# Optimization experiments

Hardware: AMD Instinct MI355X
Metric: run time of the kernel (lower is better)

The kernel has to match this reference:

```python
import jax, jax.numpy as jnp
import numpy as np

B, S, D, H, DOUT = 4, 2048, 1024, 4, 1024


def setup_inputs() -> dict:
    key = jax.random.key(0)
    ks = jax.random.split(key, 11)
    x = jax.random.normal(ks[0], (B, S, D), dtype=jnp.float32)
    phase = jax.random.normal(ks[1], (H, D), dtype=jnp.float32) * 0.02
    sc = 1.0 / np.sqrt(D)
    Wq = jax.random.normal(ks[2], (D, H * D), dtype=jnp.float32) * sc
    bq = jnp.zeros((H * D,), dtype=jnp.float32)
    Wk = jax.random.normal(ks[3], (D, H * D), dtype=jnp.float32) * sc
    bk = jnp.zeros((H * D,), dtype=jnp.float32)
    Wv = jax.random.normal(ks[4], (D, H * D), dtype=jnp.float32) * sc
    bv = jnp.zeros((H * D,), dtype=jnp.float32)
    Wo = jax.random.normal(ks[5], (H * D, DOUT), dtype=jnp.float32) / np.sqrt(H * D)
    bo = jnp.zeros((DOUT,), dtype=jnp.float32)
    return {"x": x, "phase": phase, "Wq": Wq, "bq": bq, "Wk": Wk, "bk": bk,
            "Wv": Wv, "bv": bv, "Wo": Wo, "bo": bo}


def reference(x, phase, Wq, bq, Wk, bk, Wv, bv, Wo, bo):
    b, s, d = x.shape
    h = phase.shape[0]
    q = (x @ Wq + bq).reshape(b, s, h, d)  # [B,S,H,D]
    k = (x @ Wk + bk).reshape(b, s, h, d)
    v = (x @ Wv + bv).reshape(b, s, h, d)
    # q *= e^{i phase}; k *= e^{-i phase}; scores = Re(q @ k^T) over last dim.
    # Re( e^{i p1} e^{-i p2} ) = cos(p1)cos(p2) + sin(p1)sin(p2), so use real pairs.
    c, sn = jnp.cos(phase), jnp.sin(phase)  # [H,D]
    qr, qi = q * c, q * sn
    kr, ki = k * c, k * sn
    scale = 1.0 / np.sqrt(d)
    # per-position head-vs-head scores: [B,S,H,H]
    scores = (jnp.einsum('bshd,bsgd->bshg', qr, kr)
              + jnp.einsum('bshd,bsgd->bshg', qi, ki)) * scale
    attn = jax.nn.softmax(scores, axis=-1)  # dropout is identity in eval
    out = jnp.einsum('bshg,bsgd->bshd', attn, v)  # [B,S,H,D]
    # replicate torch: transpose(1,2) -> [B,H,S,D] then view [B,S,H*D]
    out = jnp.swapaxes(out, 1, 2).reshape(b, s, h * d)
    return out @ Wo + bo
```

## Files before the change

kernel.cpp:

```cpp
#include <hip/hip_runtime.h>
#include <hip/hip_bf16.h>
#include <stdint.h>

#define DEVI __device__ __forceinline__

using f32x4  = __attribute__((ext_vector_type(4))) float;
using bf16x8 = __attribute__((ext_vector_type(8))) short;

DEVI ushort f2bf(float f) {
  union { float f; uint32_t u; } v; v.f = f;
  uint32_t u = v.u;
  uint32_t r = (u + 0x7fffu + ((u >> 16) & 1u)) >> 16;
  return (ushort)r;
}
DEVI float bf2f(ushort h) {
  union { uint32_t u; float f; } v; v.u = ((uint32_t)h) << 16;
  return v.f;
}

__global__ void k_cast_bf16(const float* __restrict__ in, ushort* __restrict__ out, int n8) {
  int i = blockIdx.x * blockDim.x + threadIdx.x;
  if (i >= n8) return;
  const float4* in4 = reinterpret_cast<const float4*>(in);
  float4 a = in4[i * 2], b = in4[i * 2 + 1];
  uint4 o;
  o.x = (uint32_t)f2bf(a.x) | ((uint32_t)f2bf(a.y) << 16);
  o.y = (uint32_t)f2bf(a.z) | ((uint32_t)f2bf(a.w) << 16);
  o.z = (uint32_t)f2bf(b.x) | ((uint32_t)f2bf(b.y) << 16);
  o.w = (uint32_t)f2bf(b.z) | ((uint32_t)f2bf(b.w) << 16);
  reinterpret_cast<uint4*>(out)[i] = o;
}

__global__ __launch_bounds__(256)
void k_transpose_cast(const float* __restrict__ in, ushort* __restrict__ out, int R, int C) {
  __shared__ float tile[64][65];
  int c0 = blockIdx.x * 64, r0 = blockIdx.y * 64;
  int t = threadIdx.x, tr = t >> 6, tc = t & 63;
#pragma unroll
  for (int i = 0; i < 16; ++i) {
    int r = i * 4 + tr;
    tile[r][tc] = in[(size_t)(r0 + r) * C + c0 + tc];
  }
  __syncthreads();
#pragma unroll
  for (int i = 0; i < 16; ++i) {
    int rr = i * 4 + tr;
    out[(size_t)(c0 + rr) * R + r0 + tc] = f2bf(tile[tc][rr]);
  }
}

__global__ void k_phase(const float* __restrict__ p, float* __restrict__ c,
                        float* __restrict__ s, int n) {
  int i = blockIdx.x * blockDim.x + threadIdx.x;
  if (i < n) { float v = p[i]; c[i] = cosf(v); s[i] = sinf(v); }
}

__global__ void k_concat3(const float* __restrict__ a, const float* __restrict__ b,
                          const float* __restrict__ c, float* __restrict__ o, int n) {
  int i = blockIdx.x * blockDim.x + threadIdx.x;
  if (i < n) { o[i] = a[i]; o[i + n] = b[i]; o[i + 2 * n] = c[i]; }
}

DEVI void glds16(const ushort* g, ushort* l) {
  __builtin_amdgcn_global_load_lds(
      (const __attribute__((address_space(1))) void*)g,
      (__attribute__((address_space(3))) void*)l, 16, 0, 0);
}

template <typename OutT>
__global__ __launch_bounds__(512, 2)
void k_gemm256(const ushort* __restrict__ A, const ushort* __restrict__ Bt,
               const float* __restrict__ bias, OutT* __restrict__ C,
               int M, int N, int K) {
  __shared__ ushort lds[3 * 16384];

  int nbx = N >> 8;
  int nwg = gridDim.x, orig = blockIdx.x;
  int bm, bn;
  if ((nbx & 7) == 0 && nbx >= 16 && (nwg & 7) == 0) {
    int xcd = orig & 7, idx = orig >> 3, sw2 = nbx >> 3;
    bm = idx / sw2;
    bn = xcd * sw2 + idx % sw2;
  } else {
    int q = nwg >> 3, r8 = nwg & 7;
    int xcd = orig & 7, idx = orig >> 3;
    int swz = (xcd < r8 ? xcd * (q + 1) : r8 * (q + 1) + (xcd - r8) * q) + idx;
    bm = swz / nbx; bn = swz % nbx;
  }

  int t = threadIdx.x;
  int lane = t & 63, wid = t >> 6;
  int wm = wid >> 2, wn = wid & 3;
  int fr = lane & 15, fq = lane >> 4;
  int spR = fq ^ ((fr >> 1) & 3);

  int rl  = t >> 2;
  int spW = (t & 3) ^ ((rl >> 1) & 3);
  const ushort* aS0 = A  + (size_t)(bm * 256 + rl) * K + spW * 8;
  const ushort* aS1 = aS0 + (size_t)128 * K;
  const ushort* bS0 = Bt + (size_t)(bn * 256 + rl) * K + spW * 8;
  const ushort* bS1 = bS0 + (size_t)128 * K;
  ushort* ldsw = lds + wid * 512;

  f32x4 acc[8][4] = {};
  int NT = K >> 5;

  glds16(aS0,      ldsw);
  glds16(aS1,      ldsw + 4096);
  glds16(bS0,      ldsw + 8192);
  glds16(bS1,      ldsw + 12288);
  glds16(aS0 + 32, ldsw + 16384);
  glds16(aS1 + 32, ldsw + 16384 + 4096);
  glds16(bS0 + 32, ldsw + 16384 + 8192);
  glds16(bS1 + 32, ldsw + 16384 + 12288);
  asm volatile("s_waitcnt vmcnt(4)" ::: "memory");
  __builtin_amdgcn_s_barrier();
  __builtin_amdgcn_sched_barrier(0);

  int iA0 = (wm * 128 + fr) * 4 + spR;
  int iB0 = (wn * 64 + fr) * 4 + spR;

  for (int kt = 0; kt < NT; ++kt) {
    if (kt + 2 < NT) {
      ushort* lb = lds + ((kt + 2) % 3) * 16384 + wid * 512;
      int ko = (kt + 2) * 32;
      glds16(aS0 + ko, lb);
      glds16(aS1 + ko, lb + 4096);
      glds16(bS0 + ko, lb + 8192);
      glds16(bS1 + ko, lb + 12288);
    }
    const bf16x8* Av = reinterpret_cast<const bf16x8*>(lds + (kt % 3) * 16384);
    const bf16x8* Bv = Av + 1024;

    bf16x8 bfr[4];
#pragma unroll
    for (int nt = 0; nt < 4; ++nt) bfr[nt] = Bv[iB0 + nt * 64];

#pragma unroll
    for (int mi = 0; mi < 2; ++mi) {
      bf16x8 af[4];
#pragma unroll
      for (int m4 = 0; m4 < 4; ++m4) af[m4] = Av[iA0 + (mi * 4 + m4) * 64];
      __builtin_amdgcn_s_setprio(1);
#pragma unroll
      for (int m4 = 0; m4 < 4; ++m4)
#pragma unroll
        for (int nt = 0; nt < 4; ++nt)
          acc[mi * 4 + m4][nt] =
              __builtin_amdgcn_mfma_f32_16x16x32_bf16(af[m4], bfr[nt], acc[mi * 4 + m4][nt], 0, 0, 0);
      __builtin_amdgcn_s_setprio(0);
    }

    if (kt + 1 < NT) {
      if (kt + 2 < NT) { asm volatile("s_waitcnt vmcnt(4)" ::: "memory"); }
      else             { asm volatile("s_waitcnt vmcnt(0)" ::: "memory"); }
      __builtin_amdgcn_s_barrier();
      __builtin_amdgcn_sched_barrier(0);
    }
  }

#pragma unroll
  for (int mt = 0; mt < 8; ++mt)
#pragma unroll
    for (int nt = 0; nt < 4; ++nt) {
      int col = bn * 256 + wn * 64 + nt * 16 + fr;
      float bb = bias[col];
#pragma unroll
      for (int i = 0; i < 4; ++i) {
        int row = bm * 256 + wm * 128 + mt * 16 + fq * 4 + i;
        float v = acc[mt][nt][i] + bb;
        size_t off = (size_t)row * N + col;
        if constexpr (sizeof(OutT) == 2) C[off] = f2bf(v);
        else                             C[off] = v;
      }
    }
}

template <typename OutT>
__global__ __launch_bounds__(512, 2)
void k_gemm_n128(const ushort* __restrict__ A, const ushort* __restrict__ Bt,
                 const float* __restrict__ bias, OutT* __restrict__ C,
                 int M, int N, int K) {
  __shared__ ushort lds[3 * 12288];

  int nbx = N >> 7;
  int nwg = gridDim.x, orig = blockIdx.x;
  int q = nwg >> 3, r8 = nwg & 7;
  int xcd = orig & 7, idx = orig >> 3;
  int swz = (xcd < r8 ? xcd * (q + 1) : r8 * (q + 1) + (xcd - r8) * q) + idx;
  int bm = swz / nbx, bn = swz % nbx;

  int t = threadIdx.x;
  int lane = t & 63, wid = t >> 6;
  int wm = wid >> 1, wn = wid & 1;
  int fr = lane & 15, fq = lane >> 4;
  int spR = fq ^ ((fr >> 1) & 3);

  int rl  = t >> 2;
  int spW = (t & 3) ^ ((rl >> 1) & 3);
  const ushort* aS0 = A  + (size_t)(bm * 256 + rl) * K + spW * 8;
  const ushort* aS1 = aS0 + (size_t)128 * K;
  const ushort* bS0 = Bt + (size_t)(bn * 128 + rl) * K + spW * 8;
  ushort* ldsw = lds + wid * 512;

  f32x4 acc[4][4] = {};
  int NT = K >> 5;

  glds16(aS0,      ldsw);
  glds16(aS1,      ldsw + 4096);
  glds16(bS0,      ldsw + 8192);
  glds16(aS0 + 32, ldsw + 12288);
  glds16(aS1 + 32, ldsw + 12288 + 4096);
  glds16(bS0 + 32, ldsw + 12288 + 8192);
  asm volatile("s_waitcnt vmcnt(3)" ::: "memory");
  __builtin_amdgcn_s_barrier();
  __builtin_amdgcn_sched_barrier(0);

  int iA0 = (wm * 64 + fr) * 4 + spR;
  int iB0 = (wn * 64 + fr) * 4 + spR;

  for (int kt = 0; kt < NT; ++kt) {
    if (kt + 2 < NT) {
      ushort* lb = lds + ((kt + 2) % 3) * 12288 + wid * 512;
      int ko = (kt + 2) * 32;
      glds16(aS0 + ko, lb);
      glds16(aS1 + ko, lb + 4096);
      glds16(bS0 + ko, lb + 8192);
    }
    const bf16x8* Av = reinterpret_cast<const bf16x8*>(lds + (kt % 3) * 12288);
    const bf16x8* Bv = Av + 1024;

    bf16x8 bfr[4], af[4];
#pragma unroll
    for (int nt = 0; nt < 4; ++nt) bfr[nt] = Bv[iB0 + nt * 64];
#pragma unroll
    for (int m4 = 0; m4 < 4; ++m4) af[m4] = Av[iA0 + m4 * 64];
    __builtin_amdgcn_s_setprio(1);
#pragma unroll
    for (int m4 = 0; m4 < 4; ++m4)
#pragma unroll
      for (int nt = 0; nt < 4; ++nt)
        acc[m4][nt] = __builtin_amdgcn_mfma_f32_16x16x32_bf16(af[m4], bfr[nt], acc[m4][nt], 0, 0, 0);
    __builtin_amdgcn_s_setprio(0);

    if (kt + 1 < NT) {
      if (kt + 2 < NT) { asm volatile("s_waitcnt vmcnt(3)" ::: "memory"); }
      else             { asm volatile("s_waitcnt vmcnt(0)" ::: "memory"); }
      __builtin_amdgcn_s_barrier();
      __builtin_amdgcn_sched_barrier(0);
    }
  }

#pragma unroll
  for (int m4 = 0; m4 < 4; ++m4)
#pragma unroll
    for (int nt = 0; nt < 4; ++nt) {
      int col = bn * 128 + wn * 64 + nt * 16 + fr;
      float bb = bias[col];
#pragma unroll
      for (int i = 0; i < 4; ++i) {
        int row = bm * 256 + wm * 64 + m4 * 16 + fq * 4 + i;
        float v = acc[m4][nt][i] + bb;
        size_t off = (size_t)row * N + col;
        if constexpr (sizeof(OutT) == 2) C[off] = f2bf(v);
        else                             C[off] = v;
      }
    }
}

__global__ __launch_bounds__(256)
void k_attn(const ushort* __restrict__ QKV, const float* __restrict__ ct,
            const float* __restrict__ st, ushort* __restrict__ Y) {
  int p = blockIdx.x;
  int t = threadIdx.x;
  int lane = t & 63, wid = t >> 6;
  int d0 = t * 4;
  __shared__ float wsc[4][16];

  float q[4][4], k[4][4], v[4][4], c[4][4], s[4][4];
  const ushort* base = QKV + (size_t)p * 12288 + d0;
#pragma unroll
  for (int h = 0; h < 4; ++h) {
    ushort4 uq = *reinterpret_cast<const ushort4*>(base + h * 1024);
    ushort4 uk = *reinterpret_cast<const ushort4*>(base + 4096 + h * 1024);
    ushort4 uv = *reinterpret_cast<const ushort4*>(base + 8192 + h * 1024);
    q[h][0] = bf2f(uq.x); q[h][1] = bf2f(uq.y); q[h][2] = bf2f(uq.z); q[h][3] = bf2f(uq.w);
    k[h][0] = bf2f(uk.x); k[h][1] = bf2f(uk.y); k[h][2] = bf2f(uk.z); k[h][3] = bf2f(uk.w);
    v[h][0] = bf2f(uv.x); v[h][1] = bf2f(uv.y); v[h][2] = bf2f(uv.z); v[h][3] = bf2f(uv.w);
    float4 fc = *reinterpret_cast<const float4*>(ct + h * 1024 + d0);
    float4 fs = *reinterpret_cast<const float4*>(st + h * 1024 + d0);
    c[h][0] = fc.x; c[h][1] = fc.y; c[h][2] = fc.z; c[h][3] = fc.w;
    s[h][0] = fs.x; s[h][1] = fs.y; s[h][2] = fs.z; s[h][3] = fs.w;
  }
  float qr[4][4], qi[4][4], kr[4][4], ki[4][4];
#pragma unroll
  for (int h = 0; h < 4; ++h)
#pragma unroll
    for (int dd = 0; dd < 4; ++dd) {
      qr[h][dd] = q[h][dd] * c[h][dd];
      qi[h][dd] = q[h][dd] * s[h][dd];
      kr[h][dd] = k[h][dd] * c[h][dd];
      ki[h][dd] = k[h][dd] * s[h][dd];
    }
  float sc[16];
#pragma unroll
  for (int h = 0; h < 4; ++h)
#pragma unroll
    for (int g = 0; g < 4; ++g) {
      float a = 0.f;
#pragma unroll
      for (int dd = 0; dd < 4; ++dd)
        a += qr[h][dd] * kr[g][dd] + qi[h][dd] * ki[g][dd];
      sc[h * 4 + g] = a;
    }
#pragma unroll
  for (int j = 0; j < 16; ++j) {
    float x = sc[j];
    for (int off = 32; off; off >>= 1) x += __shfl_xor(x, off, 64);
    sc[j] = x;
  }
  if (lane == 0) {
#pragma unroll
    for (int j = 0; j < 16; ++j) wsc[wid][j] = sc[j];
  }
  __syncthreads();
  float fsc[16];
#pragma unroll
  for (int j = 0; j < 16; ++j)
    fsc[j] = (wsc[0][j] + wsc[1][j] + wsc[2][j] + wsc[3][j]) * 0.03125f;

  float attn[4][4];
#pragma unroll
  for (int h = 0; h < 4; ++h) {
    float m = fmaxf(fmaxf(fsc[h * 4 + 0], fsc[h * 4 + 1]), fmaxf(fsc[h * 4 + 2], fsc[h * 4 + 3]));
    float e0 = __expf(fsc[h * 4 + 0] - m), e1 = __expf(fsc[h * 4 + 1] - m);
    float e2 = __expf(fsc[h * 4 + 2] - m), e3 = __expf(fsc[h * 4 + 3] - m);
    float inv = 1.f / (e0 + e1 + e2 + e3);
    attn[h][0] = e0 * inv; attn[h][1] = e1 * inv; attn[h][2] = e2 * inv; attn[h][3] = e3 * inv;
  }
  int bl = p >> 11, ss = p & 2047;
#pragma unroll
  for (int h = 0; h < 4; ++h) {
    float o[4];
#pragma unroll
    for (int dd = 0; dd < 4; ++dd)
      o[dd] = attn[h][0] * v[0][dd] + attn[h][1] * v[1][dd] +
              attn[h][2] * v[2][dd] + attn[h][3] * v[3][dd];
    ushort4 ov;
    ov.x = f2bf(o[0]); ov.y = f2bf(o[1]); ov.z = f2bf(o[2]); ov.w = f2bf(o[3]);
    *reinterpret_cast<ushort4*>(Y + ((size_t)(bl * 4 + h) * 2048 + ss) * 1024 + d0) = ov;
  }
}

extern "C" void kernel_launch(void* const* d_in, const int* in_sizes, int n_in,
                              void* d_out, int out_size, void* d_ws, size_t ws_size,
                              hipStream_t stream) {
  const float* x  = (const float*)d_in[0];
  const float* ph = (const float*)d_in[1];
  const float* Wq = (const float*)d_in[2];
  const float* bq = (const float*)d_in[3];
  const float* Wk = (const float*)d_in[4];
  const float* bk = (const float*)d_in[5];
  const float* Wv = (const float*)d_in[6];
  const float* bv = (const float*)d_in[7];
  const float* Wo = (const float*)d_in[8];
  const float* bo = (const float*)d_in[9];
  float* out = (float*)d_out;

  const int B = 4, S = 2048, D = 1024, H = 4;
  const int M = B * S;
  const int HD = H * D;
  const int N3 = 3 * HD;

  const size_t fixed = (size_t)M * D * 2
                     + (size_t)N3 * D * 2
                     + (size_t)D * HD * 2
                     + (size_t)2 * HD * 4
                     + (size_t)N3 * 4;
  int NC; bool full_y;
  if      (ws_size >= fixed + (size_t)M     * N3 * 2 + (size_t)M * HD * 2) { NC = 1; full_y = true; }
  else if (ws_size >= fixed + (size_t)(M/2) * N3 * 2 + (size_t)M * HD * 2) { NC = 2; full_y = true; }
  else if (ws_size >= fixed + (size_t)(M/4) * N3 * 2 + (size_t)M * HD * 2) { NC = 4; full_y = true; }
  else                                                                      { NC = 4; full_y = false; }
  const int Mc = M / NC;

  char* w = (char*)d_ws;
  ushort* Xb    = (ushort*)w; w += (size_t)M * D * 2;
  ushort* WqkvT = (ushort*)w; w += (size_t)N3 * D * 2;
  ushort* WoT   = (ushort*)w; w += (size_t)D * HD * 2;
  float*  ct    = (float*)w;  w += (size_t)HD * 4;
  float*  st    = (float*)w;  w += (size_t)HD * 4;
  float*  bqkv  = (float*)w;  w += (size_t)N3 * 4;
  ushort* QKVc  = (ushort*)w; w += (size_t)Mc * N3 * 2;
  ushort* Yb    = (ushort*)w; w += (size_t)(full_y ? M : Mc) * HD * 2;

  k_cast_bf16<<<(M * D / 8 + 255) / 256, 256, 0, stream>>>(x, Xb, M * D / 8);
  k_transpose_cast<<<dim3(HD / 64, D / 64), 256, 0, stream>>>(Wq, WqkvT,                    D, HD);
  k_transpose_cast<<<dim3(HD / 64, D / 64), 256, 0, stream>>>(Wk, WqkvT + (size_t)HD * D,   D, HD);
  k_transpose_cast<<<dim3(HD / 64, D / 64), 256, 0, stream>>>(Wv, WqkvT + (size_t)2*HD*D,   D, HD);
  k_transpose_cast<<<dim3(D / 64, HD / 64), 256, 0, stream>>>(Wo, WoT, HD, D);
  k_phase<<<(HD + 255) / 256, 256, 0, stream>>>(ph, ct, st, HD);
  k_concat3<<<(HD + 255) / 256, 256, 0, stream>>>(bq, bk, bv, bqkv, HD);

  for (int c = 0; c < NC; ++c) {
    const ushort* Ac = Xb + (size_t)c * Mc * D;
    k_gemm256<ushort><<<(Mc / 256) * (N3 / 256), 512, 0, stream>>>(
        Ac, WqkvT, bqkv, QKVc, Mc, N3, D);
    ushort* Yc = full_y ? (Yb + (size_t)c * Mc * HD) : Yb;
    k_attn<<<Mc, 256, 0, stream>>>(QKVc, ct, st, Yc);
    if (!full_y) {
      k_gemm_n128<float><<<(Mc / 256) * (D / 128), 512, 0, stream>>>(
          Yc, WoT, bo, out + (size_t)c * Mc * D, Mc, D, HD);
    }
  }
  if (full_y) {
    k_gemm_n128<float><<<(M / 256) * (D / 128), 512, 0, stream>>>(Yb, WoT, bo, out, M, D, HD);
  }
}
```

Baseline: 395.8 us.

## Load GEMM B operand directly from global into registers, bypassing LDS

Both GEMM kernels now stage only A through LDS. Each wave loads its B fragments straight from global memory into double-buffered registers, prefetching one k-step ahead, and the main loop is unrolled by two to swap the buffers. This cuts LDS footprint, LDS traffic and the B-side LDS reads, and the vmcnt waits are adjusted to match. B reads are now less coalesced (16-byte per lane across rows) and use more registers. The n128 kernel also gets a simple block-to-tile mapping for N=1024.

```diff
diff --git a/kernel.cpp b/kernel.cpp
--- a/kernel.cpp
+++ b/kernel.cpp
@@ -72,7 +72,7 @@
 void k_gemm256(const ushort* __restrict__ A, const ushort* __restrict__ Bt,
                const float* __restrict__ bias, OutT* __restrict__ C,
                int M, int N, int K) {
-  __shared__ ushort lds[3 * 16384];
+  __shared__ ushort lds[3 * 8192];
 
   int nbx = N >> 8;
   int nwg = gridDim.x, orig = blockIdx.x;
@@ -96,46 +96,41 @@
 
   int rl  = t >> 2;
   int spW = (t & 3) ^ ((rl >> 1) & 3);
-  const ushort* aS0 = A  + (size_t)(bm * 256 + rl) * K + spW * 8;
+  const ushort* aS0 = A + (size_t)(bm * 256 + rl) * K + spW * 8;
   const ushort* aS1 = aS0 + (size_t)128 * K;
-  const ushort* bS0 = Bt + (size_t)(bn * 256 + rl) * K + spW * 8;
-  const ushort* bS1 = bS0 + (size_t)128 * K;
   ushort* ldsw = lds + wid * 512;
+  const ushort* bP = Bt + (size_t)(bn * 256 + wn * 64 + fr) * K + fq * 8;
 
   f32x4 acc[8][4] = {};
   int NT = K >> 5;
 
+  bf16x8 b0[4], b1[4];
   glds16(aS0,      ldsw);
   glds16(aS1,      ldsw + 4096);
-  glds16(bS0,      ldsw + 8192);
-  glds16(bS1,      ldsw + 12288);
-  glds16(aS0 + 32, ldsw + 16384);
-  glds16(aS1 + 32, ldsw + 16384 + 4096);
-  glds16(bS0 + 32, ldsw + 16384 + 8192);
-  glds16(bS1 + 32, ldsw + 16384 + 12288);
-  asm volatile("s_waitcnt vmcnt(4)" ::: "memory");
+  glds16(aS0 + 32, ldsw + 8192);
+  glds16(aS1 + 32, ldsw + 8192 + 4096);
+#pragma unroll
+  for (int nt = 0; nt < 4; ++nt) b0[nt] = *reinterpret_cast<const bf16x8*>(bP + (size_t)nt * 16 * K);
+  asm volatile("s_waitcnt vmcnt(2)" ::: "memory");
   __builtin_amdgcn_s_barrier();
   __builtin_amdgcn_sched_barrier(0);
 
   int iA0 = (wm * 128 + fr) * 4 + spR;
-  int iB0 = (wn * 64 + fr) * 4 + spR;
-
-  for (int kt = 0; kt < NT; ++kt) {
+
+  auto body = [&](int kt, bf16x8 (&bc)[4], bf16x8 (&bx)[4]) {
     if (kt + 2 < NT) {
-      ushort* lb = lds + ((kt + 2) % 3) * 16384 + wid * 512;
+      ushort* lb = lds + ((kt + 2) % 3) * 8192 + wid * 512;
       int ko = (kt + 2) * 32;
       glds16(aS0 + ko, lb);
       glds16(aS1 + ko, lb + 4096);
-      glds16(bS0 + ko, lb + 8192);
-      glds16(bS1 + ko, lb + 12288);
-    }
-    const bf16x8* Av = reinterpret_cast<const bf16x8*>(lds + (kt % 3) * 16384);
-    const bf16x8* Bv = Av + 1024;
-
-    bf16x8 bfr[4];
-#pragma unroll
-    for (int nt = 0; nt < 4; ++nt) bfr[nt] = Bv[iB0 + nt * 64];
-
+    }
+    if (kt + 1 < NT) {
+      int ko = (kt + 1) * 32;
+#pragma unroll
+      for (int nt = 0; nt < 4; ++nt)
+        bx[nt] = *reinterpret_cast<const bf16x8*>(bP + (size_t)nt * 16 * K + ko);
+    }
+    const bf16x8* Av = reinterpret_cast<const bf16x8*>(lds + (kt % 3) * 8192);
 #pragma unroll
     for (int mi = 0; mi < 2; ++mi) {
       bf16x8 af[4];
@@ -147,16 +142,20 @@
 #pragma unroll
         for (int nt = 0; nt < 4; ++nt)
           acc[mi * 4 + m4][nt] =
-              __builtin_amdgcn_mfma_f32_16x16x32_bf16(af[m4], bfr[nt], acc[mi * 4 + m4][nt], 0, 0, 0);
+              __builtin_amdgcn_mfma_f32_16x16x32_bf16(af[m4], bc[nt], acc[mi * 4 + m4][nt], 0, 0, 0);
       __builtin_amdgcn_s_setprio(0);
     }
-
     if (kt + 1 < NT) {
-      if (kt + 2 < NT) { asm volatile("s_waitcnt vmcnt(4)" ::: "memory"); }
-      else             { asm volatile("s_waitcnt vmcnt(0)" ::: "memory"); }
+      if (kt + 2 < NT) { asm volatile("s_waitcnt vmcnt(6)" ::: "memory"); }
+      else             { asm volatile("s_waitcnt vmcnt(4)" ::: "memory"); }
       __builtin_amdgcn_s_barrier();
       __builtin_amdgcn_sched_barrier(0);
     }
+  };
+
+  for (int kt = 0; kt < NT; kt += 2) {
+    body(kt,     b0, b1);
+    body(kt + 1, b1, b0);
   }
 
 #pragma unroll
@@ -181,14 +180,20 @@
 void k_gemm_n128(const ushort* __restrict__ A, const ushort* __restrict__ Bt,
                  const float* __restrict__ bias, OutT* __restrict__ C,
                  int M, int N, int K) {
-  __shared__ ushort lds[3 * 12288];
+  __shared__ ushort lds[3 * 8192];
 
   int nbx = N >> 7;
   int nwg = gridDim.x, orig = blockIdx.x;
-  int q = nwg >> 3, r8 = nwg & 7;
-  int xcd = orig & 7, idx = orig >> 3;
-  int swz = (xcd < r8 ? xcd * (q + 1) : r8 * (q + 1) + (xcd - r8) * q) + idx;
-  int bm = swz / nbx, bn = swz % nbx;
+  int bm, bn;
+  if (nbx == 8 && (nwg & 7) == 0) {
+    bn = orig & 7;
+    bm = orig >> 3;
+  } else {
+    int q = nwg >> 3, r8 = nwg & 7;
+    int xcd = orig & 7, idx = orig >> 3;
+    int swz = (xcd < r8 ? xcd * (q + 1) : r8 * (q + 1) + (xcd - r8) * q) + idx;
+    bm = swz / nbx; bn = swz % nbx;
+  }
 
   int t = threadIdx.x;
   int lane = t & 63, wid = t >> 6;
@@ -198,41 +203,42 @@
 
   int rl  = t >> 2;
   int spW = (t & 3) ^ ((rl >> 1) & 3);
-  const ushort* aS0 = A  + (size_t)(bm * 256 + rl) * K + spW * 8;
+  const ushort* aS0 = A + (size_t)(bm * 256 + rl) * K + spW * 8;
   const ushort* aS1 = aS0 + (size_t)128 * K;
-  const ushort* bS0 = Bt + (size_t)(bn * 128 + rl) * K + spW * 8;
   ushort* ldsw = lds + wid * 512;
+  const ushort* bP = Bt + (size_t)(bn * 128 + wn * 64 + fr) * K + fq * 8;
 
   f32x4 acc[4][4] = {};
   int NT = K >> 5;
 
+  bf16x8 b0[4], b1[4];
   glds16(aS0,      ldsw);
   glds16(aS1,      ldsw + 4096);
-  glds16(bS0,      ldsw + 8192);
-  glds16(aS0 + 32, ldsw + 12288);
-  glds16(aS1 + 32, ldsw + 12288 + 4096);
-  glds16(bS0 + 32, ldsw + 12288 + 8192);
-  asm volatile("s_waitcnt vmcnt(3)" ::: "memory");
+  glds16(aS0 + 32, ldsw + 8192);
+  glds16(aS1 + 32, ldsw + 8192 + 4096);
+#pragma unroll
+  for (int nt = 0; nt < 4; ++nt) b0[nt] = *reinterpret_cast<const bf16x8*>(bP + (size_t)nt * 16 * K);
+  asm volatile("s_waitcnt vmcnt(2)" ::: "memory");
   __builtin_amdgcn_s_barrier();
   __builtin_amdgcn_sched_barrier(0);
 
   int iA0 = (wm * 64 + fr) * 4 + spR;
-  int iB0 = (wn * 64 + fr) * 4 + spR;
-
-  for (int kt = 0; kt < NT; ++kt) {
+
+  auto body = [&](int kt, bf16x8 (&bc)[4], bf16x8 (&bx)[4]) {
     if (kt + 2 < NT) {
-      ushort* lb = lds + ((kt + 2) % 3) * 12288 + wid * 512;
+      ushort* lb = lds + ((kt + 2) % 3) * 8192 + wid * 512;
       int ko = (kt + 2) * 32;
       glds16(aS0 + ko, lb);
       glds16(aS1 + ko, lb + 4096);
-      glds16(bS0 + ko, lb + 8192);
-    }
-    const bf16x8* Av = reinterpret_cast<const bf16x8*>(lds + (kt % 3) * 12288);
-    const bf16x8* Bv = Av + 1024;
-
-    bf16x8 bfr[4], af[4];
-#pragma unroll
-    for (int nt = 0; nt < 4; ++nt) bfr[nt] = Bv[iB0 + nt * 64];
+    }
+    if (kt + 1 < NT) {
+      int ko = (kt + 1) * 32;
+#pragma unroll
+      for (int nt = 0; nt < 4; ++nt)
+        bx[nt] = *reinterpret_cast<const bf16x8*>(bP + (size_t)nt * 16 * K + ko);
+    }
+    const bf16x8* Av = reinterpret_cast<const bf16x8*>(lds + (kt % 3) * 8192);
+    bf16x8 af[4];
 #pragma unroll
     for (int m4 = 0; m4 < 4; ++m4) af[m4] = Av[iA0 + m4 * 64];
     __builtin_amdgcn_s_setprio(1);
@@ -240,15 +246,19 @@
     for (int m4 = 0; m4 < 4; ++m4)
 #pragma unroll
       for (int nt = 0; nt < 4; ++nt)
-        acc[m4][nt] = __builtin_amdgcn_mfma_f32_16x16x32_bf16(af[m4], bfr[nt], acc[m4][nt], 0, 0, 0);
+        acc[m4][nt] = __builtin_amdgcn_mfma_f32_16x16x32_bf16(af[m4], bc[nt], acc[m4][nt], 0, 0, 0);
     __builtin_amdgcn_s_setprio(0);
-
     if (kt + 1 < NT) {
-      if (kt + 2 < NT) { asm volatile("s_waitcnt vmcnt(3)" ::: "memory"); }
-      else             { asm volatile("s_waitcnt vmcnt(0)" ::: "memory"); }
+      if (kt + 2 < NT) { asm volatile("s_waitcnt vmcnt(6)" ::: "memory"); }
+      else             { asm volatile("s_waitcnt vmcnt(4)" ::: "memory"); }
       __builtin_amdgcn_s_barrier();
       __builtin_amdgcn_sched_barrier(0);
     }
+  };
+
+  for (int kt = 0; kt < NT; kt += 2) {
+    body(kt,     b0, b1);
+    body(kt + 1, b1, b0);
   }
 
 #pragma unroll
```

Measured after the change: 574.0 us. 1.45x slower.
